# Optimization experiments

Hardware: AMD Instinct MI355X
Metric: run time of the kernel (lower is better)

Reference implementation:

```python
import jax, jax.numpy as jnp
import numpy as np

V, E, C = 50000, 5000, 16
TAU = 0.5
EPS = 1e-08
SPARSITY = 0.02  # fraction of (v,e) incidences


def setup_inputs() -> dict:
    key = jax.random.key(0)
    k1, k2, k3, k4 = jax.random.split(key, 4)
    pred_s = jax.random.normal(k1, (V, C), dtype=jnp.float32)
    pred_t = jax.random.normal(k2, (V, C), dtype=jnp.float32)
    # binary incidence matrix; pin vertex 0 into every edge so deg_e > 0
    H = (jax.random.uniform(k3, (V, E)) < SPARSITY).astype(jnp.float32)
    H = H.at[0, :].set(1.0)
    e_mask = jax.random.randint(k4, (E,), 0, 2).astype(jnp.bool_)
    return {"pred_s": pred_s, "pred_t": pred_t, "H": H, "e_mask": e_mask}


def _v2e_mean(p, H, deg_e):
    # == einsum('vc,ve->ec', p, H @ diag(1/deg_e)) : column-normalized scatter-mean
    return jnp.einsum('ve,vc->ec', H, p) / deg_e[:, None]


def reference(pred_s, pred_t, H, e_mask):
    ps = jax.nn.softmax(pred_s, axis=1)   # [V, C]
    pt = jax.nn.softmax(pred_t, axis=1)   # [V, C]
    deg_e = H.sum(axis=0)                 # [E]
    log_s = jnp.log(_v2e_mean(ps, H, deg_e) / TAU + EPS)  # [E, C]
    log_t = jnp.log(_v2e_mean(pt, H, deg_e) / TAU + EPS)  # [E, C]
    # F.kl_div(input=log_s, target=log_t, log_target=True, reduction='batchmean')
    # restricted to masked edges; mask via weights to keep shapes static.
    kl = jnp.exp(log_t) * (log_t - log_s)                  # [E, C]
    m = e_mask.astype(kl.dtype)                            # [E]
    n_sel = jnp.maximum(m.sum(), 1.0)
    return (kl * m[:, None]).sum() / n_sel
```

## Files before the change

### kernel.cpp

```cpp
#include <hip/hip_runtime.h>

#define NV 50000
#define NE 5000
#define NC 16
#define TAU_INV 2.0f
#define EPS 1e-8f
#define VCHUNK 1000
#define NCHUNK 50

__global__ __launch_bounds__(256) void softmax_kernel(
    const float* __restrict__ pred_s, const float* __restrict__ pred_t,
    float* __restrict__ p) {
  int i = blockIdx.x * 256 + threadIdx.x;
  if (i >= 2 * NV) return;
  const float* src;
  float* dst;
  if (i < NV) { src = pred_s + (size_t)i * NC; dst = p + (size_t)i * 32; }
  else        { int j = i - NV; src = pred_t + (size_t)j * NC; dst = p + (size_t)j * 32 + 16; }
  float4 a = ((const float4*)src)[0];
  float4 b = ((const float4*)src)[1];
  float4 c = ((const float4*)src)[2];
  float4 d = ((const float4*)src)[3];
  float x[16] = {a.x,a.y,a.z,a.w, b.x,b.y,b.z,b.w, c.x,c.y,c.z,c.w, d.x,d.y,d.z,d.w};
  float mx = x[0];
#pragma unroll
  for (int k = 1; k < 16; ++k) mx = fmaxf(mx, x[k]);
  float sum = 0.f;
#pragma unroll
  for (int k = 0; k < 16; ++k) { x[k] = expf(x[k] - mx); sum += x[k]; }
  float inv = 1.f / sum;
#pragma unroll
  for (int k = 0; k < 16; ++k) x[k] *= inv;
  float4 o0 = {x[0], x[1], x[2], x[3]};
  float4 o1 = {x[4], x[5], x[6], x[7]};
  float4 o2 = {x[8], x[9], x[10], x[11]};
  float4 o3 = {x[12], x[13], x[14], x[15]};
  ((float4*)dst)[0] = o0;
  ((float4*)dst)[1] = o1;
  ((float4*)dst)[2] = o2;
  ((float4*)dst)[3] = o3;
}

__global__ __launch_bounds__(256, 4) void accum_kernel(
    const float* __restrict__ H, const float* __restrict__ p,
    float* __restrict__ acc) {
  int te = blockIdx.x * 256 + threadIdx.x;
  int e = te < NE ? te : NE - 1;
  int v0 = blockIdx.y * VCHUNK;

  float deg = 0.f;
  float as[16], at[16];
#pragma unroll
  for (int k = 0; k < 16; ++k) { as[k] = 0.f; at[k] = 0.f; }

  const float* __restrict__ hp = H + (size_t)v0 * NE + e;
  const float* __restrict__ pp = p + (size_t)v0 * 32;

#pragma unroll 2
  for (int v = 0; v < VCHUNK; ++v) {
    float h = hp[(size_t)v * NE];
    float4 sA = ((const float4*)(pp + (size_t)v * 32))[0];
    float4 sB = ((const float4*)(pp + (size_t)v * 32))[1];
    float4 sC = ((const float4*)(pp + (size_t)v * 32))[2];
    float4 sD = ((const float4*)(pp + (size_t)v * 32))[3];
    float4 tA = ((const float4*)(pp + (size_t)v * 32))[4];
    float4 tB = ((const float4*)(pp + (size_t)v * 32))[5];
    float4 tC = ((const float4*)(pp + (size_t)v * 32))[6];
    float4 tD = ((const float4*)(pp + (size_t)v * 32))[7];
    float sv[16] = {sA.x,sA.y,sA.z,sA.w, sB.x,sB.y,sB.z,sB.w,
                    sC.x,sC.y,sC.z,sC.w, sD.x,sD.y,sD.z,sD.w};
    float tv[16] = {tA.x,tA.y,tA.z,tA.w, tB.x,tB.y,tB.z,tB.w,
                    tC.x,tC.y,tC.z,tC.w, tD.x,tD.y,tD.z,tD.w};
    deg += h;
#pragma unroll
    for (int k = 0; k < 16; ++k) as[k] = fmaf(h, sv[k], as[k]);
#pragma unroll
    for (int k = 0; k < 16; ++k) at[k] = fmaf(h, tv[k], at[k]);
  }

  if (te < NE) {
    atomicAdd(&acc[e], deg);
#pragma unroll
    for (int k = 0; k < 16; ++k)
      atomicAdd(&acc[NE + (size_t)k * NE + e], as[k]);
#pragma unroll
    for (int k = 0; k < 16; ++k)
      atomicAdd(&acc[(size_t)17 * NE + (size_t)k * NE + e], at[k]);
  }
}

__global__ __launch_bounds__(256) void kl_kernel(
    const float* __restrict__ acc, const unsigned char* __restrict__ e_mask,
    float* __restrict__ out) {
  __shared__ float snum[4];
  __shared__ float scnt[4];
  int t = threadIdx.x;
  float num = 0.f, cnt = 0.f;
  for (int e = t; e < NE; e += 256) {
    if (e_mask[e]) {
      float deg = acc[e];
      float invd = 1.f / deg;
      float kl = 0.f;
#pragma unroll
      for (int k = 0; k < 16; ++k) {
        float ms = acc[NE + (size_t)k * NE + e] * invd;
        float mt = acc[(size_t)17 * NE + (size_t)k * NE + e] * invd;
        float xs = ms * TAU_INV + EPS;
        float xt = mt * TAU_INV + EPS;
        kl += xt * (logf(xt) - logf(xs));
      }
      num += kl;
      cnt += 1.f;
    }
  }
#pragma unroll
  for (int off = 32; off > 0; off >>= 1) {
    num += __shfl_down(num, off, 64);
    cnt += __shfl_down(cnt, off, 64);
  }
  if ((t & 63) == 0) { snum[t >> 6] = num; scnt[t >> 6] = cnt; }
  __syncthreads();
  if (t == 0) {
    float n = snum[0] + snum[1] + snum[2] + snum[3];
    float c2 = scnt[0] + scnt[1] + scnt[2] + scnt[3];
    out[0] = n / fmaxf(c2, 1.f);
  }
}

extern "C" void kernel_launch(void* const* d_in, const int* in_sizes, int n_in,
                              void* d_out, int out_size, void* d_ws, size_t ws_size,
                              hipStream_t stream) {
  const float* pred_s = (const float*)d_in[0];
  const float* pred_t = (const float*)d_in[1];
  const float* H      = (const float*)d_in[2];
  const unsigned char* e_mask = (const unsigned char*)d_in[3];

  float* ws = (float*)d_ws;
  float* p   = ws;
  float* acc = ws + (size_t)NV * 32;

  hipMemsetAsync(acc, 0, (size_t)33 * NE * sizeof(float), stream);
  softmax_kernel<<<dim3((2 * NV + 255) / 256), 256, 0, stream>>>(pred_s, pred_t, p);
  accum_kernel<<<dim3((NE + 255) / 256, NCHUNK), 256, 0, stream>>>(H, p, acc);
  kl_kernel<<<1, 256, 0, stream>>>(acc, e_mask, (float*)d_out);
}
```

Measured before the change: 1.448 ms.

## Compact H into per-chunk nonzero index lists and gather only incident vertices

Replaces the dense accumulation over every (vertex, edge) pair with two kernels. A sparsify pass scans H once and records the indices of nonzero vertices per edge lane and per vertex chunk, capped at 64. A gather pass then sums the softmax rows of only those vertices and uses the count as the degree. This removes the dense multiply-add work over mostly-zero entries but assumes H is binary, and it silently drops incidences if a chunk has more than 64.

```diff
diff --git a/kernel.cpp b/kernel.cpp
--- a/kernel.cpp
+++ b/kernel.cpp
@@ -7,6 +7,8 @@
 #define EPS 1e-8f
 #define VCHUNK 1000
 #define NCHUNK 50
+#define NLANE 5120
+#define CAP 64
 
 __global__ __launch_bounds__(256) void softmax_kernel(
     const float* __restrict__ pred_s, const float* __restrict__ pred_t,
@@ -41,51 +43,65 @@
   ((float4*)dst)[3] = o3;
 }
 
-__global__ __launch_bounds__(256, 4) void accum_kernel(
-    const float* __restrict__ H, const float* __restrict__ p,
-    float* __restrict__ acc) {
+__global__ __launch_bounds__(256, 4) void sparsify_kernel(
+    const float* __restrict__ H, int* __restrict__ nz, int* __restrict__ cnts) {
   int te = blockIdx.x * 256 + threadIdx.x;
   int e = te < NE ? te : NE - 1;
-  int v0 = blockIdx.y * VCHUNK;
+  int y = blockIdx.y;
+  int v0 = y * VCHUNK;
+  const float* __restrict__ hp = H + (size_t)v0 * NE + e;
+  int* __restrict__ mybuf = nz + (size_t)y * CAP * NLANE + te;
+  int cnt = 0;
+  for (int vb = 0; vb < VCHUNK; vb += 8) {
+    float h[8];
+#pragma unroll
+    for (int u = 0; u < 8; ++u) h[u] = hp[(size_t)(vb + u) * NE];
+#pragma unroll
+    for (int u = 0; u < 8; ++u) {
+      if (h[u] != 0.0f && cnt < CAP) {
+        mybuf[(size_t)cnt * NLANE] = v0 + vb + u;
+        cnt++;
+      }
+    }
+  }
+  cnts[y * NLANE + te] = cnt;
+}
 
-  float deg = 0.f;
+__global__ __launch_bounds__(256, 4) void gather_kernel(
+    const int* __restrict__ nz, const int* __restrict__ cnts,
+    const float* __restrict__ p, float* __restrict__ acc) {
+  int te = blockIdx.x * 256 + threadIdx.x;
+  int y = blockIdx.y;
+  int cnt = (te < NE) ? cnts[y * NLANE + te] : 0;
+  const int* __restrict__ mybuf = nz + (size_t)y * CAP * NLANE + te;
+
   float as[16], at[16];
 #pragma unroll
   for (int k = 0; k < 16; ++k) { as[k] = 0.f; at[k] = 0.f; }
 
-  const float* __restrict__ hp = H + (size_t)v0 * NE + e;
-  const float* __restrict__ pp = p + (size_t)v0 * 32;
-
-#pragma unroll 2
-  for (int v = 0; v < VCHUNK; ++v) {
-    float h = hp[(size_t)v * NE];
-    float4 sA = ((const float4*)(pp + (size_t)v * 32))[0];
-    float4 sB = ((const float4*)(pp + (size_t)v * 32))[1];
-    float4 sC = ((const float4*)(pp + (size_t)v * 32))[2];
-    float4 sD = ((const float4*)(pp + (size_t)v * 32))[3];
-    float4 tA = ((const float4*)(pp + (size_t)v * 32))[4];
-    float4 tB = ((const float4*)(pp + (size_t)v * 32))[5];
-    float4 tC = ((const float4*)(pp + (size_t)v * 32))[6];
-    float4 tD = ((const float4*)(pp + (size_t)v * 32))[7];
-    float sv[16] = {sA.x,sA.y,sA.z,sA.w, sB.x,sB.y,sB.z,sB.w,
-                    sC.x,sC.y,sC.z,sC.w, sD.x,sD.y,sD.z,sD.w};
-    float tv[16] = {tA.x,tA.y,tA.z,tA.w, tB.x,tB.y,tB.z,tB.w,
-                    tC.x,tC.y,tC.z,tC.w, tD.x,tD.y,tD.z,tD.w};
-    deg += h;
-#pragma unroll
-    for (int k = 0; k < 16; ++k) as[k] = fmaf(h, sv[k], as[k]);
-#pragma unroll
-    for (int k = 0; k < 16; ++k) at[k] = fmaf(h, tv[k], at[k]);
+  for (int j = 0; j < cnt; ++j) {
+    int v = mybuf[(size_t)j * NLANE];
+    const float4* __restrict__ r = (const float4*)(p + (size_t)v * 32);
+    float4 sA = r[0], sB = r[1], sC = r[2], sD = r[3];
+    float4 tA = r[4], tB = r[5], tC = r[6], tD = r[7];
+    as[0] += sA.x;  as[1] += sA.y;  as[2] += sA.z;  as[3] += sA.w;
+    as[4] += sB.x;  as[5] += sB.y;  as[6] += sB.z;  as[7] += sB.w;
+    as[8] += sC.x;  as[9] += sC.y;  as[10] += sC.z; as[11] += sC.w;
+    as[12] += sD.x; as[13] += sD.y; as[14] += sD.z; as[15] += sD.w;
+    at[0] += tA.x;  at[1] += tA.y;  at[2] += tA.z;  at[3] += tA.w;
+    at[4] += tB.x;  at[5] += tB.y;  at[6] += tB.z;  at[7] += tB.w;
+    at[8] += tC.x;  at[9] += tC.y;  at[10] += tC.z; at[11] += tC.w;
+    at[12] += tD.x; at[13] += tD.y; at[14] += tD.z; at[15] += tD.w;
   }
 
   if (te < NE) {
-    atomicAdd(&acc[e], deg);
+    atomicAdd(&acc[te], (float)cnt);
 #pragma unroll
     for (int k = 0; k < 16; ++k)
-      atomicAdd(&acc[NE + (size_t)k * NE + e], as[k]);
+      atomicAdd(&acc[NE + (size_t)k * NE + te], as[k]);
 #pragma unroll
     for (int k = 0; k < 16; ++k)
-      atomicAdd(&acc[(size_t)17 * NE + (size_t)k * NE + e], at[k]);
+      atomicAdd(&acc[(size_t)17 * NE + (size_t)k * NE + te], at[k]);
   }
 }
 
@@ -135,12 +151,15 @@
   const float* H      = (const float*)d_in[2];
   const unsigned char* e_mask = (const unsigned char*)d_in[3];
 
-  float* ws = (float*)d_ws;
+  float* ws  = (float*)d_ws;
   float* p   = ws;
   float* acc = ws + (size_t)NV * 32;
+  int*  cnts = (int*)(acc + (size_t)33 * NE);
+  int*  nz   = cnts + (size_t)NCHUNK * NLANE;
 
   hipMemsetAsync(acc, 0, (size_t)33 * NE * sizeof(float), stream);
   softmax_kernel<<<dim3((2 * NV + 255) / 256), 256, 0, stream>>>(pred_s, pred_t, p);
-  accum_kernel<<<dim3((NE + 255) / 256, NCHUNK), 256, 0, stream>>>(H, p, acc);
+  sparsify_kernel<<<dim3(NLANE / 256, NCHUNK), 256, 0, stream>>>(H, nz, cnts);
+  gather_kernel<<<dim3(NLANE / 256, NCHUNK), 256, 0, stream>>>(nz, cnts, p, acc);
   kl_kernel<<<1, 256, 0, stream>>>(acc, e_mask, (float*)d_out);
 }
```

Result: slower. 1.523 ms (+5.2%).

## Register-tile four edges per thread and replace atomics with partial-sum reduction

Applied to the files above, without the earlier changes.

Each accumulation thread now owns four consecutive edges, loading H as float4 and reusing every broadcast softmax row across four edges. H rows are software-prefetched one vertex group ahead. Atomic accumulation and the memset are replaced by per-chunk partial buffers and a separate reduce kernel. The aim is to cut per-FMA load-instruction overhead on p, at the cost of high register pressure (132 accumulators, 2 blocks per CU), a small grid of 500 blocks, and extra partial-buffer traffic.

```diff
diff --git a/kernel.cpp b/kernel.cpp
--- a/kernel.cpp
+++ b/kernel.cpp
@@ -5,8 +5,12 @@
 #define NC 16
 #define TAU_INV 2.0f
 #define EPS 1e-8f
-#define VCHUNK 1000
-#define NCHUNK 50
+
+#define NLANE 5120
+#define EBLK 1024
+#define NXB 5
+#define NCH 100
+#define VCH 500
 
 __global__ __launch_bounds__(256) void softmax_kernel(
     const float* __restrict__ pred_s, const float* __restrict__ pred_t,
@@ -41,52 +45,83 @@
   ((float4*)dst)[3] = o3;
 }
 
-__global__ __launch_bounds__(256, 4) void accum_kernel(
+__global__ __launch_bounds__(256, 2) void accum_kernel(
     const float* __restrict__ H, const float* __restrict__ p,
-    float* __restrict__ acc) {
-  int te = blockIdx.x * 256 + threadIdx.x;
-  int e = te < NE ? te : NE - 1;
-  int v0 = blockIdx.y * VCHUNK;
+    float* __restrict__ part) {
+  int xb = blockIdx.x;
+  int y  = blockIdx.y;
+  int e0 = xb * EBLK + 4 * (int)threadIdx.x;
+  if (e0 > NE - 4) e0 = NE - 4;
+  int v0 = y * VCH;
 
-  float deg = 0.f;
-  float as[16], at[16];
+  float4 aS[16], aT[16], dg;
 #pragma unroll
-  for (int k = 0; k < 16; ++k) { as[k] = 0.f; at[k] = 0.f; }
+  for (int k = 0; k < 16; ++k) {
+    aS[k] = make_float4(0.f, 0.f, 0.f, 0.f);
+    aT[k] = make_float4(0.f, 0.f, 0.f, 0.f);
+  }
+  dg = make_float4(0.f, 0.f, 0.f, 0.f);
 
-  const float* __restrict__ hp = H + (size_t)v0 * NE + e;
-  const float* __restrict__ pp = p + (size_t)v0 * 32;
+  const float* __restrict__ hbase = H + (size_t)v0 * NE + e0;
+  const float* __restrict__ pbase = p + (size_t)v0 * 32;
 
-#pragma unroll 2
-  for (int v = 0; v < VCHUNK; ++v) {
-    float h = hp[(size_t)v * NE];
-    float4 sA = ((const float4*)(pp + (size_t)v * 32))[0];
-    float4 sB = ((const float4*)(pp + (size_t)v * 32))[1];
-    float4 sC = ((const float4*)(pp + (size_t)v * 32))[2];
-    float4 sD = ((const float4*)(pp + (size_t)v * 32))[3];
-    float4 tA = ((const float4*)(pp + (size_t)v * 32))[4];
-    float4 tB = ((const float4*)(pp + (size_t)v * 32))[5];
-    float4 tC = ((const float4*)(pp + (size_t)v * 32))[6];
-    float4 tD = ((const float4*)(pp + (size_t)v * 32))[7];
-    float sv[16] = {sA.x,sA.y,sA.z,sA.w, sB.x,sB.y,sB.z,sB.w,
-                    sC.x,sC.y,sC.z,sC.w, sD.x,sD.y,sD.z,sD.w};
-    float tv[16] = {tA.x,tA.y,tA.z,tA.w, tB.x,tB.y,tB.z,tB.w,
-                    tC.x,tC.y,tC.z,tC.w, tD.x,tD.y,tD.z,tD.w};
-    deg += h;
+  float4 hc[4];
 #pragma unroll
-    for (int k = 0; k < 16; ++k) as[k] = fmaf(h, sv[k], as[k]);
+  for (int u = 0; u < 4; ++u)
+    hc[u] = *(const float4*)(hbase + (size_t)u * NE);
+
+  for (int vb = 0; vb < VCH; vb += 4) {
+    int nb = (vb + 4 < VCH) ? vb + 4 : vb;
+    float4 hn[4];
 #pragma unroll
-    for (int k = 0; k < 16; ++k) at[k] = fmaf(h, tv[k], at[k]);
+    for (int u = 0; u < 4; ++u)
+      hn[u] = *(const float4*)(hbase + (size_t)(nb + u) * NE);
+
+#pragma unroll
+    for (int u = 0; u < 4; ++u) {
+      const float4* __restrict__ r = (const float4*)(pbase + (size_t)(vb + u) * 32);
+      float4 s0 = r[0], s1 = r[1], s2 = r[2], s3 = r[3];
+      float4 t0 = r[4], t1 = r[5], t2 = r[6], t3 = r[7];
+      float4 h = hc[u];
+      dg.x += h.x; dg.y += h.y; dg.z += h.z; dg.w += h.w;
+      float sv[16] = {s0.x,s0.y,s0.z,s0.w, s1.x,s1.y,s1.z,s1.w,
+                      s2.x,s2.y,s2.z,s2.w, s3.x,s3.y,s3.z,s3.w};
+      float tv[16] = {t0.x,t0.y,t0.z,t0.w, t1.x,t1.y,t1.z,t1.w,
+                      t2.x,t2.y,t2.z,t2.w, t3.x,t3.y,t3.z,t3.w};
+#pragma unroll
+      for (int k = 0; k < 16; ++k) {
+        aS[k].x = fmaf(h.x, sv[k], aS[k].x);
+        aS[k].y = fmaf(h.y, sv[k], aS[k].y);
+        aS[k].z = fmaf(h.z, sv[k], aS[k].z);
+        aS[k].w = fmaf(h.w, sv[k], aS[k].w);
+        aT[k].x = fmaf(h.x, tv[k], aT[k].x);
+        aT[k].y = fmaf(h.y, tv[k], aT[k].y);
+        aT[k].z = fmaf(h.z, tv[k], aT[k].z);
+        aT[k].w = fmaf(h.w, tv[k], aT[k].w);
+      }
+    }
+#pragma unroll
+    for (int u = 0; u < 4; ++u) hc[u] = hn[u];
   }
 
-  if (te < NE) {
-    atomicAdd(&acc[e], deg);
+  float* op = part + (size_t)y * 33 * NLANE + e0;
 #pragma unroll
-    for (int k = 0; k < 16; ++k)
-      atomicAdd(&acc[NE + (size_t)k * NE + e], as[k]);
+  for (int k = 0; k < 16; ++k)
+    *(float4*)(op + (size_t)k * NLANE) = aS[k];
 #pragma unroll
-    for (int k = 0; k < 16; ++k)
-      atomicAdd(&acc[(size_t)17 * NE + (size_t)k * NE + e], at[k]);
-  }
+  for (int k = 0; k < 16; ++k)
+    *(float4*)(op + (size_t)(16 + k) * NLANE) = aT[k];
+  *(float4*)(op + (size_t)32 * NLANE) = dg;
+}
+
+__global__ __launch_bounds__(256) void reduce_kernel(
+    const float* __restrict__ part, float* __restrict__ acc) {
+  int i = blockIdx.x * 256 + threadIdx.x;
+  if (i >= 33 * NLANE) return;
+  float s = 0.f;
+#pragma unroll 4
+  for (int y = 0; y < NCH; ++y) s += part[(size_t)y * 33 * NLANE + i];
+  acc[i] = s;
 }
 
 __global__ __launch_bounds__(256) void kl_kernel(
@@ -98,13 +133,13 @@
   float num = 0.f, cnt = 0.f;
   for (int e = t; e < NE; e += 256) {
     if (e_mask[e]) {
-      float deg = acc[e];
+      float deg = acc[(size_t)32 * NLANE + e];
       float invd = 1.f / deg;
       float kl = 0.f;
 #pragma unroll
       for (int k = 0; k < 16; ++k) {
-        float ms = acc[NE + (size_t)k * NE + e] * invd;
-        float mt = acc[(size_t)17 * NE + (size_t)k * NE + e] * invd;
+        float ms = acc[(size_t)k * NLANE + e] * invd;
+        float mt = acc[(size_t)(16 + k) * NLANE + e] * invd;
         float xs = ms * TAU_INV + EPS;
         float xt = mt * TAU_INV + EPS;
         kl += xt * (logf(xt) - logf(xs));
@@ -135,12 +170,13 @@
   const float* H      = (const float*)d_in[2];
   const unsigned char* e_mask = (const unsigned char*)d_in[3];
 
-  float* ws = (float*)d_ws;
-  float* p   = ws;
-  float* acc = ws + (size_t)NV * 32;
+  float* ws   = (float*)d_ws;
+  float* p    = ws;
+  float* acc  = ws + (size_t)NV * 32;
+  float* part = acc + (size_t)33 * NLANE;
 
-  hipMemsetAsync(acc, 0, (size_t)33 * NE * sizeof(float), stream);
   softmax_kernel<<<dim3((2 * NV + 255) / 256), 256, 0, stream>>>(pred_s, pred_t, p);
-  accum_kernel<<<dim3((NE + 255) / 256, NCHUNK), 256, 0, stream>>>(H, p, acc);
+  accum_kernel<<<dim3(NXB, NCH), 256, 0, stream>>>(H, p, part);
+  reduce_kernel<<<dim3((33 * NLANE + 255) / 256), 256, 0, stream>>>(part, acc);
   kl_kernel<<<1, 256, 0, stream>>>(acc, e_mask, (float*)d_out);
 }
```

New measurement: 1.428 ms. No clear change (-1.4%).
